# Performance work log

Measured on AMD Instinct MI355X. Metric: run time of the kernel, lower is better.

## Reference

```python
import math
import jax, jax.numpy as jnp
import numpy as np

DIM = 192
HEADS = 6
WIN = (16, 16)
N = WIN[0] * WIN[1]
B_ = 256
NW = 64
CPB_HIDDEN = 512


def _relative_coords_table(window_size):
    Wh, Ww = window_size
    h = np.arange(-(Wh - 1), Wh, dtype=np.float32)
    w = np.arange(-(Ww - 1), Ww, dtype=np.float32)
    table = np.stack(np.meshgrid(h, w, indexing='ij'), axis=-1)[None]  # (1, 2Wh-1, 2Ww-1, 2)
    table[..., 0] /= (Wh - 1)
    table[..., 1] /= (Ww - 1)
    table *= 8.0
    table = np.sign(table) * np.log2(np.abs(table) + 1.0) / np.log2(8.0)
    return table.astype(np.float32)


def _relative_position_index(window_size):
    Wh, Ww = window_size
    coords = np.stack(np.meshgrid(np.arange(Wh), np.arange(Ww), indexing='ij'))  # (2, Wh, Ww)
    flat = coords.reshape(2, -1)
    rel = flat[:, :, None] - flat[:, None, :]  # (2, N, N)
    rel = rel.transpose(1, 2, 0).astype(np.int64)
    rel[..., 0] += Wh - 1
    rel[..., 1] += Ww - 1
    rel[..., 0] *= 2 * Ww - 1
    return rel.sum(-1)  # (N, N)


def setup_inputs() -> dict:
    key = jax.random.key(0)
    ks = jax.random.split(key, 9)
    s = 1.0 / math.sqrt(DIM)
    inp = {
        'x': jax.random.normal(ks[0], (B_, N, DIM), dtype=jnp.float32),
        'mask': jax.random.normal(ks[1], (NW, N, N), dtype=jnp.float32),
        'qkv_w': jax.random.normal(ks[2], (3 * DIM, DIM), dtype=jnp.float32) * s,
        'qkv_b': jnp.zeros((3 * DIM,), dtype=jnp.float32),
        'proj_w': jax.random.normal(ks[3], (DIM, DIM), dtype=jnp.float32) * s,
        'proj_b': jnp.zeros((DIM,), dtype=jnp.float32),
        'logit_scale': jnp.full((HEADS, 1, 1), math.log(10.0), dtype=jnp.float32),
        'cpb_w1': jax.random.normal(ks[4], (CPB_HIDDEN, 2), dtype=jnp.float32) * (1.0 / math.sqrt(2.0)),
        'cpb_b1': jnp.zeros((CPB_HIDDEN,), dtype=jnp.float32),
        'cpb_w2': jax.random.normal(ks[5], (HEADS, CPB_HIDDEN), dtype=jnp.float32) * (1.0 / math.sqrt(CPB_HIDDEN)),
        'coords_table': jnp.asarray(_relative_coords_table(WIN)),
        'rel_index': jnp.asarray(_relative_position_index(WIN)),
    }
    return inp


def reference(x, mask, qkv_w, qkv_b, proj_w, proj_b, logit_scale,
              cpb_w1, cpb_b1, cpb_w2, coords_table, rel_index):
    Bw, n, C = x.shape
    H = logit_scale.shape[0]
    Dh = C // H
    eps = 1e-12

    qkv = x @ qkv_w.T + qkv_b                             # (B_, N, 3C)
    qkv = qkv.reshape(Bw, n, 3, H, Dh).transpose(2, 0, 3, 1, 4)
    q, k, v = qkv[0], qkv[1], qkv[2]                      # (B_, H, N, Dh)

    qn = q / jnp.maximum(jnp.linalg.norm(q, axis=-1, keepdims=True), eps)
    kn = k / jnp.maximum(jnp.linalg.norm(k, axis=-1, keepdims=True), eps)
    attn = jnp.einsum('bhnd,bhmd->bhnm', qn, kn)

    scale = jnp.exp(jnp.minimum(logit_scale, math.log(1.0 / 0.01)))  # (H,1,1)
    attn = attn * scale[None]

    # CPB MLP bias: (1, 2Wh-1, 2Ww-1, 2) -> (-1, H), gather, sigmoid-scale
    hbt = jax.nn.relu(coords_table @ cpb_w1.T + cpb_b1) @ cpb_w2.T   # (1, 2Wh-1, 2Ww-1, H)
    bias_table = hbt.reshape(-1, H)
    bias = bias_table[rel_index.reshape(-1)].reshape(n, n, H).transpose(2, 0, 1)
    attn = attn + 16.0 * jax.nn.sigmoid(bias)[None]

    nW = mask.shape[0]
    attn = attn.reshape(Bw // nW, nW, H, n, n) + mask[None, :, None]
    attn = attn.reshape(Bw, H, n, n)

    attn = jax.nn.softmax(attn, axis=-1)
    out = jnp.einsum('bhnm,bhmd->bhnd', attn, v)
    out = out.transpose(0, 2, 1, 3).reshape(Bw, n, C)
    return out @ proj_w.T + proj_b
```

## Files before the change

kernel.cpp:

```cpp
#include <hip/hip_runtime.h>

using bf16 = __bf16;
typedef bf16 bf16x4 __attribute__((ext_vector_type(4)));
typedef bf16 bf16x8 __attribute__((ext_vector_type(8)));
typedef float f32x4 __attribute__((ext_vector_type(4)));

__device__ __forceinline__ int swz192(int row, int col) {
  return row * 192 + (col ^ ((row & 7) << 3));
}
__device__ __forceinline__ int qk_idx(int row, int col) {
  return (row >> 1) * 64 + (row & 1) * 32 + (col ^ (((row >> 1) & 3) << 3));
}
__device__ __forceinline__ int vt_idx(int d, int n) {
  return d * 256 + (((n + ((d >> 3) << 4)) & 255) ^ ((d & 7) << 3));
}
__device__ __forceinline__ int p_idx4(int wv, int r, int c) {
  return wv * 1024 + r * 64 + (c ^ ((r & 7) << 3));
}

#define LOG2E 1.44269504088896f

template <bool A_BF16, bool OUT_F32, bool NORM_QK, int NT>
__global__ __launch_bounds__(256) void k_gemm(const void* __restrict__ Ap,
                                              const float* __restrict__ W,
                                              const float* __restrict__ bias,
                                              const float* __restrict__ lsc,
                                              void* __restrict__ Op, int Ntot) {
  __shared__ bf16 As[128 * 192];
  __shared__ bf16 Bs[64 * 192];
  const int bid = blockIdx.x;
  const int xcd = bid & 7;
  const int j = bid >> 3;
  const int m0 = (xcd + 8 * (j / NT)) * 128;
  const int n0 = (j % NT) * 64;
  const int t = threadIdx.x;

  if (A_BF16) {
    const bf16* A = (const bf16*)Ap;
#pragma unroll
    for (int i = 0; i < 12; ++i) {
      int f = t + i * 256;
      int row = f / 24, c8 = f % 24;
      bf16x8 v = *reinterpret_cast<const bf16x8*>(&A[(m0 + row) * 192 + c8 * 8]);
      *reinterpret_cast<bf16x8*>(&As[swz192(row, c8 * 8)]) = v;
    }
  } else {
    const float* A = (const float*)Ap;
#pragma unroll
    for (int i = 0; i < 24; ++i) {
      int f = t + i * 256;
      int row = f / 48, c4 = f % 48;
      f32x4 v = *reinterpret_cast<const f32x4*>(&A[(m0 + row) * 192 + c4 * 4]);
      bf16x4 hv;
      hv[0] = (bf16)v[0]; hv[1] = (bf16)v[1]; hv[2] = (bf16)v[2]; hv[3] = (bf16)v[3];
      *reinterpret_cast<bf16x4*>(&As[swz192(row, c4 * 4)]) = hv;
    }
  }
#pragma unroll
  for (int i = 0; i < 12; ++i) {
    int f = t + i * 256;
    int row = f / 48, c4 = f % 48;
    f32x4 v = *reinterpret_cast<const f32x4*>(&W[(n0 + row) * 192 + c4 * 4]);
    bf16x4 hv;
    hv[0] = (bf16)v[0]; hv[1] = (bf16)v[1]; hv[2] = (bf16)v[2]; hv[3] = (bf16)v[3];
    *reinterpret_cast<bf16x4*>(&Bs[swz192(row, c4 * 4)]) = hv;
  }
  __syncthreads();

  const int w = t >> 6, lane = t & 63, lo = lane & 15, hi = lane >> 4;
  const int wm = (w >> 1) * 64, wn = (w & 1) * 32;
  f32x4 acc[4][2];
#pragma unroll
  for (int a = 0; a < 4; ++a)
#pragma unroll
    for (int c = 0; c < 2; ++c) acc[a][c] = f32x4{0.f, 0.f, 0.f, 0.f};

#pragma unroll
  for (int ks = 0; ks < 6; ++ks) {
    const int k0 = ks * 32 + hi * 8;
    bf16x8 af[4], bfr[2];
#pragma unroll
    for (int ri = 0; ri < 4; ++ri)
      af[ri] = *reinterpret_cast<const bf16x8*>(&As[swz192(wm + ri * 16 + lo, k0)]);
#pragma unroll
    for (int ci = 0; ci < 2; ++ci)
      bfr[ci] = *reinterpret_cast<const bf16x8*>(&Bs[swz192(wn + ci * 16 + lo, k0)]);
#pragma unroll
    for (int ri = 0; ri < 4; ++ri)
#pragma unroll
      for (int ci = 0; ci < 2; ++ci)
        acc[ri][ci] = __builtin_amdgcn_mfma_f32_16x16x32_bf16(af[ri], bfr[ci], acc[ri][ci], 0, 0, 0);
  }

  if (NORM_QK) {
    const int cb = n0 + wn;
    const bool donorm = (cb < 384);
    float smul = 1.f;
    if (cb < 192)
      smul = expf(fminf(lsc[cb >> 5], 4.605170185988091f)) * LOG2E;
    const int col0 = cb + lo;
    const float b0 = bias[col0], b1 = bias[col0 + 16];
    bf16* O = (bf16*)Op;
#pragma unroll
    for (int ri = 0; ri < 4; ++ri)
#pragma unroll
      for (int rr = 0; rr < 4; ++rr) {
        float v0 = acc[ri][0][rr] + b0;
        float v1 = acc[ri][1][rr] + b1;
        if (donorm) {
          float ss = v0 * v0 + v1 * v1;
          ss += __shfl_xor(ss, 1, 16);
          ss += __shfl_xor(ss, 2, 16);
          ss += __shfl_xor(ss, 4, 16);
          ss += __shfl_xor(ss, 8, 16);
          const float rn = smul / fmaxf(sqrtf(ss), 1e-12f);
          v0 *= rn;
          v1 *= rn;
        }
        const int row = m0 + wm + ri * 16 + hi * 4 + rr;
        O[row * Ntot + col0] = (bf16)v0;
        O[row * Ntot + col0 + 16] = (bf16)v1;
      }
  } else {
#pragma unroll
    for (int ri = 0; ri < 4; ++ri)
#pragma unroll
      for (int ci = 0; ci < 2; ++ci) {
        const int col = n0 + wn + ci * 16 + lo;
        const float bv = bias[col];
#pragma unroll
        for (int rr = 0; rr < 4; ++rr) {
          const int row = m0 + wm + ri * 16 + hi * 4 + rr;
          const float val = acc[ri][ci][rr] + bv;
          if (OUT_F32)
            __builtin_nontemporal_store(val, &((float*)Op)[row * Ntot + col]);
          else
            ((bf16*)Op)[row * Ntot + col] = (bf16)val;
        }
      }
  }
}

__global__ void k_cpb1(const float* __restrict__ ct, const float* __restrict__ w1,
                       const float* __restrict__ b1, const float* __restrict__ w2,
                       float* __restrict__ bt) {
  int idx = blockIdx.x * 256 + threadIdx.x;
  if (idx >= 961 * 6) return;
  int r = idx / 6, hh = idx % 6;
  float t0 = ct[r * 2], t1 = ct[r * 2 + 1];
  float acc = 0.f;
  for (int j = 0; j < 512; ++j) {
    float hv = fmaf(w1[j * 2], t0, fmaf(w1[j * 2 + 1], t1, b1[j]));
    hv = fmaxf(hv, 0.f);
    acc = fmaf(hv, w2[hh * 512 + j], acc);
  }
  bt[idx] = acc;
}

__global__ void k_cpbT(const float* __restrict__ bt, const int* __restrict__ rel,
                       float* __restrict__ biasfT) {
  int idx = blockIdx.x * 256 + threadIdx.x;
  int hh = idx >> 16;
  int jj = (idx >> 8) & 255;
  int i = idx & 255;
  float v = bt[rel[i * 256 + jj] * 6 + hh];
  biasfT[idx] = LOG2E * 16.f / (1.f + expf(-v));
}

__global__ __launch_bounds__(256) void k_maskT(const float* __restrict__ m,
                                               bf16* __restrict__ o) {
  __shared__ float tile[64][65];
  const int mb = blockIdx.y;
  const int it = blockIdx.x >> 2, jt = blockIdx.x & 3;
  const int tx = threadIdx.x & 63, ty = threadIdx.x >> 6;
  const float* mp = m + mb * 65536;
#pragma unroll
  for (int rr = 0; rr < 16; ++rr)
    tile[rr * 4 + ty][tx] = mp[(it * 64 + rr * 4 + ty) * 256 + jt * 64 + tx];
  __syncthreads();
  bf16* op = o + mb * 65536;
#pragma unroll
  for (int rr = 0; rr < 16; ++rr)
    op[(jt * 64 + rr * 4 + ty) * 256 + it * 64 + tx] = (bf16)(LOG2E * tile[tx][rr * 4 + ty]);
}

__global__ __launch_bounds__(256) void k_attn(const bf16* __restrict__ qkv,
                                              const bf16* __restrict__ maskT,
                                              const float* __restrict__ biasfT,
                                              bf16* __restrict__ aout) {
  __shared__ bf16 ksh[256 * 32];
  __shared__ bf16 vts[32 * 256];
  __shared__ bf16 ps[4 * 16 * 64];

  const int bid = blockIdx.x;
  const int x = bid & 7, i = bid >> 3;
  const int mb = x * 8 + i / 24;
  const int rem = i % 24;
  const int b = (rem / 6) * 64 + mb;
  const int h = rem % 6;
  const int t = threadIdx.x;

  const int rsub = t >> 2;
  const int c4 = t & 3;
#pragma unroll
  for (int p = 0; p < 4; ++p) {
    const int row = p * 64 + rsub;
    const int base = (b * 256 + row) * 576 + h * 32 + c4 * 8;
    *reinterpret_cast<bf16x8*>(&ksh[qk_idx(row, c4 * 8)]) =
        *reinterpret_cast<const bf16x8*>(&qkv[base + 192]);
    bf16x8 v = *reinterpret_cast<const bf16x8*>(&qkv[base + 384]);
#pragma unroll
    for (int j = 0; j < 8; ++j) vts[vt_idx(c4 * 8 + j, row)] = v[j];
  }
  __syncthreads();

  const int w = t >> 6, lane = t & 63, lo = lane & 15, hi = lane >> 4;
  const float* bT = biasfT + (h << 16);
  const bf16* mT = maskT + (mb << 16);
  const bf16* qbase = qkv + (b * 256) * 576 + h * 32;

  bf16x8 afn = *reinterpret_cast<const bf16x8*>(&qbase[(w * 16 + lo) * 576 + hi * 8]);

  f32x4 bvp[4];
  bf16x4 mvp[4];
  {
    const int rbase0 = w * 16 + hi * 4;
#pragma unroll
    for (int c = 0; c < 4; ++c) {
      const int col = c * 16 + lo;
      bvp[c] = *reinterpret_cast<const f32x4*>(&bT[col * 256 + rbase0]);
      mvp[c] = *reinterpret_cast<const bf16x4*>(&mT[col * 256 + rbase0]);
    }
  }

  for (int rgi = 0; rgi < 4; ++rgi) {
    const int rg = rgi * 4 + w;
    const int rbase = rg * 16 + hi * 4;
    const bf16x8 af = afn;
    if (rgi < 3)
      afn = *reinterpret_cast<const bf16x8*>(&qbase[((rg + 4) * 16 + lo) * 576 + hi * 8]);

    f32x4 po0 = {0.f, 0.f, 0.f, 0.f}, po1 = {0.f, 0.f, 0.f, 0.f};
    float sum[4] = {0.f, 0.f, 0.f, 0.f};

#pragma unroll
    for (int ph = 0; ph < 4; ++ph) {
      f32x4 bv[4];
      bf16x4 mv[4];
#pragma unroll
      for (int c = 0; c < 4; ++c) { bv[c] = bvp[c]; mv[c] = mvp[c]; }
      if (ph < 3) {
#pragma unroll
        for (int c = 0; c < 4; ++c) {
          const int col = (ph + 1) * 64 + c * 16 + lo;
          bvp[c] = *reinterpret_cast<const f32x4*>(&bT[col * 256 + rbase]);
          mvp[c] = *reinterpret_cast<const bf16x4*>(&mT[col * 256 + rbase]);
        }
      } else if (rgi < 3) {
#pragma unroll
        for (int c = 0; c < 4; ++c) {
          const int col = c * 16 + lo;
          bvp[c] = *reinterpret_cast<const f32x4*>(&bT[col * 256 + rbase + 64]);
          mvp[c] = *reinterpret_cast<const bf16x4*>(&mT[col * 256 + rbase + 64]);
        }
      }
      bf16x8 kf[4];
#pragma unroll
      for (int c4i = 0; c4i < 4; ++c4i) {
        const int ct = ph * 4 + c4i;
        kf[c4i] = *reinterpret_cast<const bf16x8*>(&ksh[qk_idx(ct * 16 + lo, hi * 8)]);
      }
      f32x4 a[4];
#pragma unroll
      for (int c4i = 0; c4i < 4; ++c4i) {
        f32x4 z = {0.f, 0.f, 0.f, 0.f};
        a[c4i] = __builtin_amdgcn_mfma_f32_16x16x32_bf16(af, kf[c4i], z, 0, 0, 0);
      }
#pragma unroll
      for (int c4i = 0; c4i < 4; ++c4i)
#pragma unroll
        for (int rr = 0; rr < 4; ++rr) {
          const float s = a[c4i][rr] + bv[c4i][rr] + (float)mv[c4i][rr];
          const float p = exp2f(s);
          sum[rr] += p;
          ps[p_idx4(w, hi * 4 + rr, c4i * 16 + lo)] = (bf16)p;
        }
#pragma unroll
      for (int kb = 0; kb < 2; ++kb) {
        const bf16x8 pa = *reinterpret_cast<const bf16x8*>(&ps[p_idx4(w, lo, kb * 32 + hi * 8)]);
        const bf16x8 b0 = *reinterpret_cast<const bf16x8*>(&vts[vt_idx(lo, ph * 64 + kb * 32 + hi * 8)]);
        const bf16x8 b1 = *reinterpret_cast<const bf16x8*>(&vts[vt_idx(16 + lo, ph * 64 + kb * 32 + hi * 8)]);
        po0 = __builtin_amdgcn_mfma_f32_16x16x32_bf16(pa, b0, po0, 0, 0, 0);
        po1 = __builtin_amdgcn_mfma_f32_16x16x32_bf16(pa, b1, po1, 0, 0, 0);
      }
    }
#pragma unroll
    for (int rr = 0; rr < 4; ++rr) {
      float s = sum[rr];
      s += __shfl_xor(s, 1, 16);
      s += __shfl_xor(s, 2, 16);
      s += __shfl_xor(s, 4, 16);
      s += __shfl_xor(s, 8, 16);
      sum[rr] = 1.f / s;
    }
#pragma unroll
    for (int rr = 0; rr < 4; ++rr) {
      const int ob = (b * 256 + rbase + rr) * 192 + h * 32;
      aout[ob + lo] = (bf16)(po0[rr] * sum[rr]);
      aout[ob + 16 + lo] = (bf16)(po1[rr] * sum[rr]);
    }
  }
}

extern "C" void kernel_launch(void* const* d_in, const int* in_sizes, int n_in,
                              void* d_out, int out_size, void* d_ws, size_t ws_size,
                              hipStream_t stream) {
  const float* x      = (const float*)d_in[0];
  const float* mask   = (const float*)d_in[1];
  const float* qkv_w  = (const float*)d_in[2];
  const float* qkv_b  = (const float*)d_in[3];
  const float* proj_w = (const float*)d_in[4];
  const float* proj_b = (const float*)d_in[5];
  const float* lsc    = (const float*)d_in[6];
  const float* cpb_w1 = (const float*)d_in[7];
  const float* cpb_b1 = (const float*)d_in[8];
  const float* cpb_w2 = (const float*)d_in[9];
  const float* ctab   = (const float*)d_in[10];
  const int*   relidx = (const int*)d_in[11];

  char* ws = (char*)d_ws;
  bf16*  qkvb   = (bf16*)(ws);
  bf16*  aoutb  = (bf16*)(ws + 75497472);
  float* biasfT = (float*)(ws + 100663296);
  bf16*  maskTb = (bf16*)(ws + 102236160);
  float* bt     = (float*)(ws + 110624768);

  k_gemm<false, false, true, 9><<<4608, 256, 0, stream>>>(x, qkv_w, qkv_b, lsc, qkvb, 576);
  k_cpb1<<<23, 256, 0, stream>>>(ctab, cpb_w1, cpb_b1, cpb_w2, bt);
  k_cpbT<<<1536, 256, 0, stream>>>(bt, relidx, biasfT);
  k_maskT<<<dim3(16, 64), 256, 0, stream>>>(mask, maskTb);
  k_attn<<<1536, 256, 0, stream>>>(qkvb, maskTb, biasfT, aoutb);
  k_gemm<true, true, false, 3><<<1536, 256, 0, stream>>>(aoutb, proj_w, proj_b, nullptr,
                                                         (float*)d_out, 192);
}
```

Measured before the change: 225.9 us.

## Compute transposed scores with MFMA accumulator bias, drop mask/bias transposes, shrink GEMM tiles

The attention kernel now computes S^T via swapped MFMA operands and feeds bias plus mask in as the accumulator input, so the mask and bias tables can stay in natural row-major layout. The shared-memory transpose kernel for the mask is replaced by a simple elementwise conversion. Probability stores become vectorised bf16x4, and the row-sum reduction becomes a cross-lane shuffle. Separately, both GEMMs use 64-row M tiles instead of 128, doubling the grid. This trades less data reuse per block for more parallelism and lower LDS use.

```diff
diff --git a/kernel.cpp b/kernel.cpp
--- a/kernel.cpp
+++ b/kernel.cpp
@@ -26,19 +26,19 @@
                                               const float* __restrict__ bias,
                                               const float* __restrict__ lsc,
                                               void* __restrict__ Op, int Ntot) {
-  __shared__ bf16 As[128 * 192];
+  __shared__ bf16 As[64 * 192];
   __shared__ bf16 Bs[64 * 192];
   const int bid = blockIdx.x;
   const int xcd = bid & 7;
   const int j = bid >> 3;
-  const int m0 = (xcd + 8 * (j / NT)) * 128;
+  const int m0 = (xcd + 8 * (j / NT)) * 64;
   const int n0 = (j % NT) * 64;
   const int t = threadIdx.x;
 
   if (A_BF16) {
     const bf16* A = (const bf16*)Ap;
 #pragma unroll
-    for (int i = 0; i < 12; ++i) {
+    for (int i = 0; i < 6; ++i) {
       int f = t + i * 256;
       int row = f / 24, c8 = f % 24;
       bf16x8 v = *reinterpret_cast<const bf16x8*>(&A[(m0 + row) * 192 + c8 * 8]);
@@ -47,7 +47,7 @@
   } else {
     const float* A = (const float*)Ap;
 #pragma unroll
-    for (int i = 0; i < 24; ++i) {
+    for (int i = 0; i < 12; ++i) {
       int f = t + i * 256;
       int row = f / 48, c4 = f % 48;
       f32x4 v = *reinterpret_cast<const f32x4*>(&A[(m0 + row) * 192 + c4 * 4]);
@@ -68,25 +68,25 @@
   __syncthreads();
 
   const int w = t >> 6, lane = t & 63, lo = lane & 15, hi = lane >> 4;
-  const int wm = (w >> 1) * 64, wn = (w & 1) * 32;
-  f32x4 acc[4][2];
-#pragma unroll
-  for (int a = 0; a < 4; ++a)
+  const int wm = (w >> 1) * 32, wn = (w & 1) * 32;
+  f32x4 acc[2][2];
+#pragma unroll
+  for (int a = 0; a < 2; ++a)
 #pragma unroll
     for (int c = 0; c < 2; ++c) acc[a][c] = f32x4{0.f, 0.f, 0.f, 0.f};
 
 #pragma unroll
   for (int ks = 0; ks < 6; ++ks) {
     const int k0 = ks * 32 + hi * 8;
-    bf16x8 af[4], bfr[2];
-#pragma unroll
-    for (int ri = 0; ri < 4; ++ri)
+    bf16x8 af[2], bfr[2];
+#pragma unroll
+    for (int ri = 0; ri < 2; ++ri)
       af[ri] = *reinterpret_cast<const bf16x8*>(&As[swz192(wm + ri * 16 + lo, k0)]);
 #pragma unroll
     for (int ci = 0; ci < 2; ++ci)
       bfr[ci] = *reinterpret_cast<const bf16x8*>(&Bs[swz192(wn + ci * 16 + lo, k0)]);
 #pragma unroll
-    for (int ri = 0; ri < 4; ++ri)
+    for (int ri = 0; ri < 2; ++ri)
 #pragma unroll
       for (int ci = 0; ci < 2; ++ci)
         acc[ri][ci] = __builtin_amdgcn_mfma_f32_16x16x32_bf16(af[ri], bfr[ci], acc[ri][ci], 0, 0, 0);
@@ -102,7 +102,7 @@
     const float b0 = bias[col0], b1 = bias[col0 + 16];
     bf16* O = (bf16*)Op;
 #pragma unroll
-    for (int ri = 0; ri < 4; ++ri)
+    for (int ri = 0; ri < 2; ++ri)
 #pragma unroll
       for (int rr = 0; rr < 4; ++rr) {
         float v0 = acc[ri][0][rr] + b0;
@@ -123,7 +123,7 @@
       }
   } else {
 #pragma unroll
-    for (int ri = 0; ri < 4; ++ri)
+    for (int ri = 0; ri < 2; ++ri)
 #pragma unroll
       for (int ci = 0; ci < 2; ++ci) {
         const int col = n0 + wn + ci * 16 + lo;
@@ -157,36 +157,23 @@
   bt[idx] = acc;
 }
 
-__global__ void k_cpbT(const float* __restrict__ bt, const int* __restrict__ rel,
-                       float* __restrict__ biasfT) {
+__global__ void k_cpb2(const float* __restrict__ bt, const int* __restrict__ rel,
+                       float* __restrict__ biasf) {
   int idx = blockIdx.x * 256 + threadIdx.x;
   int hh = idx >> 16;
-  int jj = (idx >> 8) & 255;
-  int i = idx & 255;
-  float v = bt[rel[i * 256 + jj] * 6 + hh];
-  biasfT[idx] = LOG2E * 16.f / (1.f + expf(-v));
-}
-
-__global__ __launch_bounds__(256) void k_maskT(const float* __restrict__ m,
-                                               bf16* __restrict__ o) {
-  __shared__ float tile[64][65];
-  const int mb = blockIdx.y;
-  const int it = blockIdx.x >> 2, jt = blockIdx.x & 3;
-  const int tx = threadIdx.x & 63, ty = threadIdx.x >> 6;
-  const float* mp = m + mb * 65536;
-#pragma unroll
-  for (int rr = 0; rr < 16; ++rr)
-    tile[rr * 4 + ty][tx] = mp[(it * 64 + rr * 4 + ty) * 256 + jt * 64 + tx];
-  __syncthreads();
-  bf16* op = o + mb * 65536;
-#pragma unroll
-  for (int rr = 0; rr < 16; ++rr)
-    op[(jt * 64 + rr * 4 + ty) * 256 + it * 64 + tx] = (bf16)(LOG2E * tile[tx][rr * 4 + ty]);
+  int ij = idx & 65535;
+  float v = bt[rel[ij] * 6 + hh];
+  biasf[idx] = LOG2E * 16.f / (1.f + expf(-v));
+}
+
+__global__ void k_maskb(const float* __restrict__ m, bf16* __restrict__ o) {
+  int i = blockIdx.x * 256 + threadIdx.x;
+  o[i] = (bf16)(LOG2E * m[i]);
 }
 
 __global__ __launch_bounds__(256) void k_attn(const bf16* __restrict__ qkv,
-                                              const bf16* __restrict__ maskT,
-                                              const float* __restrict__ biasfT,
+                                              const bf16* __restrict__ maskb,
+                                              const float* __restrict__ biasf,
                                               bf16* __restrict__ aout) {
   __shared__ bf16 ksh[256 * 32];
   __shared__ bf16 vts[32 * 256];
@@ -201,67 +188,70 @@
   const int t = threadIdx.x;
 
   const int rsub = t >> 2;
-  const int c4 = t & 3;
+  const int c4s = t & 3;
 #pragma unroll
   for (int p = 0; p < 4; ++p) {
     const int row = p * 64 + rsub;
-    const int base = (b * 256 + row) * 576 + h * 32 + c4 * 8;
-    *reinterpret_cast<bf16x8*>(&ksh[qk_idx(row, c4 * 8)]) =
+    const int base = (b * 256 + row) * 576 + h * 32 + c4s * 8;
+    *reinterpret_cast<bf16x8*>(&ksh[qk_idx(row, c4s * 8)]) =
         *reinterpret_cast<const bf16x8*>(&qkv[base + 192]);
     bf16x8 v = *reinterpret_cast<const bf16x8*>(&qkv[base + 384]);
 #pragma unroll
-    for (int j = 0; j < 8; ++j) vts[vt_idx(c4 * 8 + j, row)] = v[j];
+    for (int jj = 0; jj < 8; ++jj) vts[vt_idx(c4s * 8 + jj, row)] = v[jj];
   }
   __syncthreads();
 
   const int w = t >> 6, lane = t & 63, lo = lane & 15, hi = lane >> 4;
-  const float* bT = biasfT + (h << 16);
-  const bf16* mT = maskT + (mb << 16);
+  const float* bT = biasf + (h << 16);
+  const bf16* mT = maskb + (mb << 16);
   const bf16* qbase = qkv + (b * 256) * 576 + h * 32;
+  const int kofs = 4 * hi;
 
   bf16x8 afn = *reinterpret_cast<const bf16x8*>(&qbase[(w * 16 + lo) * 576 + hi * 8]);
 
   f32x4 bvp[4];
   bf16x4 mvp[4];
   {
-    const int rbase0 = w * 16 + hi * 4;
+    const int qr0 = w * 16 + lo;
 #pragma unroll
     for (int c = 0; c < 4; ++c) {
-      const int col = c * 16 + lo;
-      bvp[c] = *reinterpret_cast<const f32x4*>(&bT[col * 256 + rbase0]);
-      mvp[c] = *reinterpret_cast<const bf16x4*>(&mT[col * 256 + rbase0]);
+      bvp[c] = *reinterpret_cast<const f32x4*>(&bT[qr0 * 256 + c * 16 + kofs]);
+      mvp[c] = *reinterpret_cast<const bf16x4*>(&mT[qr0 * 256 + c * 16 + kofs]);
     }
   }
 
   for (int rgi = 0; rgi < 4; ++rgi) {
     const int rg = rgi * 4 + w;
-    const int rbase = rg * 16 + hi * 4;
+    const int qrow = rg * 16 + lo;
     const bf16x8 af = afn;
     if (rgi < 3)
       afn = *reinterpret_cast<const bf16x8*>(&qbase[((rg + 4) * 16 + lo) * 576 + hi * 8]);
 
     f32x4 po0 = {0.f, 0.f, 0.f, 0.f}, po1 = {0.f, 0.f, 0.f, 0.f};
-    float sum[4] = {0.f, 0.f, 0.f, 0.f};
+    float psum = 0.f;
 
 #pragma unroll
     for (int ph = 0; ph < 4; ++ph) {
-      f32x4 bv[4];
-      bf16x4 mv[4];
-#pragma unroll
-      for (int c = 0; c < 4; ++c) { bv[c] = bvp[c]; mv[c] = mvp[c]; }
+      f32x4 cin[4];
+#pragma unroll
+      for (int c = 0; c < 4; ++c) {
+        cin[c][0] = bvp[c][0] + (float)mvp[c][0];
+        cin[c][1] = bvp[c][1] + (float)mvp[c][1];
+        cin[c][2] = bvp[c][2] + (float)mvp[c][2];
+        cin[c][3] = bvp[c][3] + (float)mvp[c][3];
+      }
       if (ph < 3) {
 #pragma unroll
         for (int c = 0; c < 4; ++c) {
-          const int col = (ph + 1) * 64 + c * 16 + lo;
-          bvp[c] = *reinterpret_cast<const f32x4*>(&bT[col * 256 + rbase]);
-          mvp[c] = *reinterpret_cast<const bf16x4*>(&mT[col * 256 + rbase]);
+          const int k0 = (ph + 1) * 64 + c * 16 + kofs;
+          bvp[c] = *reinterpret_cast<const f32x4*>(&bT[qrow * 256 + k0]);
+          mvp[c] = *reinterpret_cast<const bf16x4*>(&mT[qrow * 256 + k0]);
         }
       } else if (rgi < 3) {
 #pragma unroll
         for (int c = 0; c < 4; ++c) {
-          const int col = c * 16 + lo;
-          bvp[c] = *reinterpret_cast<const f32x4*>(&bT[col * 256 + rbase + 64]);
-          mvp[c] = *reinterpret_cast<const bf16x4*>(&mT[col * 256 + rbase + 64]);
+          bvp[c] = *reinterpret_cast<const f32x4*>(&bT[(qrow + 64) * 256 + c * 16 + kofs]);
+          mvp[c] = *reinterpret_cast<const bf16x4*>(&mT[(qrow + 64) * 256 + c * 16 + kofs]);
         }
       }
       bf16x8 kf[4];
@@ -272,19 +262,19 @@
       }
       f32x4 a[4];
 #pragma unroll
+      for (int c4i = 0; c4i < 4; ++c4i)
+        a[c4i] = __builtin_amdgcn_mfma_f32_16x16x32_bf16(kf[c4i], af, cin[c4i], 0, 0, 0);
+#pragma unroll
       for (int c4i = 0; c4i < 4; ++c4i) {
-        f32x4 z = {0.f, 0.f, 0.f, 0.f};
-        a[c4i] = __builtin_amdgcn_mfma_f32_16x16x32_bf16(af, kf[c4i], z, 0, 0, 0);
-      }
-#pragma unroll
-      for (int c4i = 0; c4i < 4; ++c4i)
+        bf16x4 hv;
 #pragma unroll
         for (int rr = 0; rr < 4; ++rr) {
-          const float s = a[c4i][rr] + bv[c4i][rr] + (float)mv[c4i][rr];
-          const float p = exp2f(s);
-          sum[rr] += p;
-          ps[p_idx4(w, hi * 4 + rr, c4i * 16 + lo)] = (bf16)p;
-        }
+          const float p = exp2f(a[c4i][rr]);
+          psum += p;
+          hv[rr] = (bf16)p;
+        }
+        *reinterpret_cast<bf16x4*>(&ps[p_idx4(w, lo, c4i * 16 + kofs)]) = hv;
+      }
 #pragma unroll
       for (int kb = 0; kb < 2; ++kb) {
         const bf16x8 pa = *reinterpret_cast<const bf16x8*>(&ps[p_idx4(w, lo, kb * 32 + hi * 8)]);
@@ -294,20 +284,17 @@
         po1 = __builtin_amdgcn_mfma_f32_16x16x32_bf16(pa, b1, po1, 0, 0, 0);
       }
     }
+    float s = psum;
+    s += __shfl_xor(s, 16, 64);
+    s += __shfl_xor(s, 32, 64);
+    s = 1.f / s;
+    const int rbase = rg * 16 + hi * 4;
 #pragma unroll
     for (int rr = 0; rr < 4; ++rr) {
-      float s = sum[rr];
-      s += __shfl_xor(s, 1, 16);
-      s += __shfl_xor(s, 2, 16);
-      s += __shfl_xor(s, 4, 16);
-      s += __shfl_xor(s, 8, 16);
-      sum[rr] = 1.f / s;
-    }
-#pragma unroll
-    for (int rr = 0; rr < 4; ++rr) {
+      const float rs = __shfl(s, 4 * hi + rr, 64);
       const int ob = (b * 256 + rbase + rr) * 192 + h * 32;
-      aout[ob + lo] = (bf16)(po0[rr] * sum[rr]);
-      aout[ob + 16 + lo] = (bf16)(po1[rr] * sum[rr]);
+      aout[ob + lo] = (bf16)(po0[rr] * rs);
+      aout[ob + 16 + lo] = (bf16)(po1[rr] * rs);
     }
   }
 }
@@ -329,17 +316,17 @@
   const int*   relidx = (const int*)d_in[11];
 
   char* ws = (char*)d_ws;
-  bf16*  qkvb   = (bf16*)(ws);
-  bf16*  aoutb  = (bf16*)(ws + 75497472);
-  float* biasfT = (float*)(ws + 100663296);
-  bf16*  maskTb = (bf16*)(ws + 102236160);
-  float* bt     = (float*)(ws + 110624768);
-
-  k_gemm<false, false, true, 9><<<4608, 256, 0, stream>>>(x, qkv_w, qkv_b, lsc, qkvb, 576);
+  bf16*  qkvb  = (bf16*)(ws);
+  bf16*  aoutb = (bf16*)(ws + 75497472);
+  float* biasf = (float*)(ws + 100663296);
+  bf16*  maskb = (bf16*)(ws + 102236160);
+  float* bt    = (float*)(ws + 110624768);
+
+  k_gemm<false, false, true, 9><<<9216, 256, 0, stream>>>(x, qkv_w, qkv_b, lsc, qkvb, 576);
   k_cpb1<<<23, 256, 0, stream>>>(ctab, cpb_w1, cpb_b1, cpb_w2, bt);
-  k_cpbT<<<1536, 256, 0, stream>>>(bt, relidx, biasfT);
-  k_maskT<<<dim3(16, 64), 256, 0, stream>>>(mask, maskTb);
-  k_attn<<<1536, 256, 0, stream>>>(qkvb, maskTb, biasfT, aoutb);
-  k_gemm<true, true, false, 3><<<1536, 256, 0, stream>>>(aoutb, proj_w, proj_b, nullptr,
+  k_cpb2<<<1536, 256, 0, stream>>>(bt, relidx, biasf);
+  k_maskb<<<16384, 256, 0, stream>>>(mask, maskb);
+  k_attn<<<1536, 256, 0, stream>>>(qkvb, maskb, biasf, aoutb);
+  k_gemm<true, true, false, 3><<<3072, 256, 0, stream>>>(aoutb, proj_w, proj_b, nullptr,
                                                          (float*)d_out, 192);
 }
```

Measured after the change: 234.7 us. +3.9%, slower.

## Pre-convert inputs and weights to bf16 and halve GEMM M-tile

Applied to the files above, without the earlier changes.

Adds a separate conversion kernel that casts x, qkv_w and proj_w to bf16 once, so both GEMMs load bf16 operands directly instead of converting fp32 in every tile. The GEMM M-tile shrinks from 128 to 64 rows, which doubles the grid size and cuts LDS and register use per block. The cost is an extra full pass over x, writing a bf16 copy and reading it back, plus three more launches. The smaller tiles also re-read the weight tile more often.

```diff
diff --git a/kernel.cpp b/kernel.cpp
--- a/kernel.cpp
+++ b/kernel.cpp
@@ -20,73 +20,67 @@
 
 #define LOG2E 1.44269504088896f
 
-template <bool A_BF16, bool OUT_F32, bool NORM_QK, int NT>
-__global__ __launch_bounds__(256) void k_gemm(const void* __restrict__ Ap,
-                                              const float* __restrict__ W,
+__global__ void k_conv8(const float* __restrict__ in, bf16* __restrict__ o) {
+  const int i = (blockIdx.x * 256 + threadIdx.x) * 8;
+  const f32x4 a = *reinterpret_cast<const f32x4*>(&in[i]);
+  const f32x4 b = *reinterpret_cast<const f32x4*>(&in[i + 4]);
+  bf16x8 v;
+  v[0] = (bf16)a[0]; v[1] = (bf16)a[1]; v[2] = (bf16)a[2]; v[3] = (bf16)a[3];
+  v[4] = (bf16)b[0]; v[5] = (bf16)b[1]; v[6] = (bf16)b[2]; v[7] = (bf16)b[3];
+  *reinterpret_cast<bf16x8*>(&o[i]) = v;
+}
+
+template <bool OUT_F32, bool NORM_QK, int NT>
+__global__ __launch_bounds__(256) void k_gemm(const bf16* __restrict__ A,
+                                              const bf16* __restrict__ W,
                                               const float* __restrict__ bias,
                                               const float* __restrict__ lsc,
                                               void* __restrict__ Op, int Ntot) {
-  __shared__ bf16 As[128 * 192];
+  __shared__ bf16 As[64 * 192];
   __shared__ bf16 Bs[64 * 192];
   const int bid = blockIdx.x;
   const int xcd = bid & 7;
   const int j = bid >> 3;
-  const int m0 = (xcd + 8 * (j / NT)) * 128;
+  const int m0 = (xcd + 8 * (j / NT)) * 64;
   const int n0 = (j % NT) * 64;
   const int t = threadIdx.x;
 
-  if (A_BF16) {
-    const bf16* A = (const bf16*)Ap;
-#pragma unroll
-    for (int i = 0; i < 12; ++i) {
-      int f = t + i * 256;
-      int row = f / 24, c8 = f % 24;
-      bf16x8 v = *reinterpret_cast<const bf16x8*>(&A[(m0 + row) * 192 + c8 * 8]);
-      *reinterpret_cast<bf16x8*>(&As[swz192(row, c8 * 8)]) = v;
-    }
-  } else {
-    const float* A = (const float*)Ap;
-#pragma unroll
-    for (int i = 0; i < 24; ++i) {
-      int f = t + i * 256;
-      int row = f / 48, c4 = f % 48;
-      f32x4 v = *reinterpret_cast<const f32x4*>(&A[(m0 + row) * 192 + c4 * 4]);
-      bf16x4 hv;
-      hv[0] = (bf16)v[0]; hv[1] = (bf16)v[1]; hv[2] = (bf16)v[2]; hv[3] = (bf16)v[3];
-      *reinterpret_cast<bf16x4*>(&As[swz192(row, c4 * 4)]) = hv;
-    }
-  }
-#pragma unroll
-  for (int i = 0; i < 12; ++i) {
+#pragma unroll
+  for (int i = 0; i < 6; ++i) {
     int f = t + i * 256;
-    int row = f / 48, c4 = f % 48;
-    f32x4 v = *reinterpret_cast<const f32x4*>(&W[(n0 + row) * 192 + c4 * 4]);
-    bf16x4 hv;
-    hv[0] = (bf16)v[0]; hv[1] = (bf16)v[1]; hv[2] = (bf16)v[2]; hv[3] = (bf16)v[3];
-    *reinterpret_cast<bf16x4*>(&Bs[swz192(row, c4 * 4)]) = hv;
+    int row = f / 24, c8 = f % 24;
+    bf16x8 v = *reinterpret_cast<const bf16x8*>(&A[(m0 + row) * 192 + c8 * 8]);
+    *reinterpret_cast<bf16x8*>(&As[swz192(row, c8 * 8)]) = v;
+  }
+#pragma unroll
+  for (int i = 0; i < 6; ++i) {
+    int f = t + i * 256;
+    int row = f / 24, c8 = f % 24;
+    bf16x8 v = *reinterpret_cast<const bf16x8*>(&W[(n0 + row) * 192 + c8 * 8]);
+    *reinterpret_cast<bf16x8*>(&Bs[swz192(row, c8 * 8)]) = v;
   }
   __syncthreads();
 
   const int w = t >> 6, lane = t & 63, lo = lane & 15, hi = lane >> 4;
-  const int wm = (w >> 1) * 64, wn = (w & 1) * 32;
-  f32x4 acc[4][2];
-#pragma unroll
-  for (int a = 0; a < 4; ++a)
+  const int wm = (w >> 1) * 32, wn = (w & 1) * 32;
+  f32x4 acc[2][2];
+#pragma unroll
+  for (int a = 0; a < 2; ++a)
 #pragma unroll
     for (int c = 0; c < 2; ++c) acc[a][c] = f32x4{0.f, 0.f, 0.f, 0.f};
 
 #pragma unroll
   for (int ks = 0; ks < 6; ++ks) {
     const int k0 = ks * 32 + hi * 8;
-    bf16x8 af[4], bfr[2];
-#pragma unroll
-    for (int ri = 0; ri < 4; ++ri)
+    bf16x8 af[2], bfr[2];
+#pragma unroll
+    for (int ri = 0; ri < 2; ++ri)
       af[ri] = *reinterpret_cast<const bf16x8*>(&As[swz192(wm + ri * 16 + lo, k0)]);
 #pragma unroll
     for (int ci = 0; ci < 2; ++ci)
       bfr[ci] = *reinterpret_cast<const bf16x8*>(&Bs[swz192(wn + ci * 16 + lo, k0)]);
 #pragma unroll
-    for (int ri = 0; ri < 4; ++ri)
+    for (int ri = 0; ri < 2; ++ri)
 #pragma unroll
       for (int ci = 0; ci < 2; ++ci)
         acc[ri][ci] = __builtin_amdgcn_mfma_f32_16x16x32_bf16(af[ri], bfr[ci], acc[ri][ci], 0, 0, 0);
@@ -102,7 +96,7 @@
     const float b0 = bias[col0], b1 = bias[col0 + 16];
     bf16* O = (bf16*)Op;
 #pragma unroll
-    for (int ri = 0; ri < 4; ++ri)
+    for (int ri = 0; ri < 2; ++ri)
 #pragma unroll
       for (int rr = 0; rr < 4; ++rr) {
         float v0 = acc[ri][0][rr] + b0;
@@ -123,7 +117,7 @@
       }
   } else {
 #pragma unroll
-    for (int ri = 0; ri < 4; ++ri)
+    for (int ri = 0; ri < 2; ++ri)
 #pragma unroll
       for (int ci = 0; ci < 2; ++ci) {
         const int col = n0 + wn + ci * 16 + lo;
@@ -201,16 +195,16 @@
   const int t = threadIdx.x;
 
   const int rsub = t >> 2;
-  const int c4 = t & 3;
+  const int c4s = t & 3;
 #pragma unroll
   for (int p = 0; p < 4; ++p) {
     const int row = p * 64 + rsub;
-    const int base = (b * 256 + row) * 576 + h * 32 + c4 * 8;
-    *reinterpret_cast<bf16x8*>(&ksh[qk_idx(row, c4 * 8)]) =
+    const int base = (b * 256 + row) * 576 + h * 32 + c4s * 8;
+    *reinterpret_cast<bf16x8*>(&ksh[qk_idx(row, c4s * 8)]) =
         *reinterpret_cast<const bf16x8*>(&qkv[base + 192]);
     bf16x8 v = *reinterpret_cast<const bf16x8*>(&qkv[base + 384]);
 #pragma unroll
-    for (int j = 0; j < 8; ++j) vts[vt_idx(c4 * 8 + j, row)] = v[j];
+    for (int jj = 0; jj < 8; ++jj) vts[vt_idx(c4s * 8 + jj, row)] = v[jj];
   }
   __syncthreads();
 
@@ -330,16 +324,22 @@
 
   char* ws = (char*)d_ws;
   bf16*  qkvb   = (bf16*)(ws);
+  bf16*  xb     = (bf16*)(ws + 75497472);
   bf16*  aoutb  = (bf16*)(ws + 75497472);
   float* biasfT = (float*)(ws + 100663296);
   bf16*  maskTb = (bf16*)(ws + 102236160);
   float* bt     = (float*)(ws + 110624768);
-
-  k_gemm<false, false, true, 9><<<4608, 256, 0, stream>>>(x, qkv_w, qkv_b, lsc, qkvb, 576);
+  bf16*  qkv_wb = (bf16*)(ws + 110647840);
+  bf16*  proj_wb= (bf16*)(ws + 110869024);
+
+  k_conv8<<<6144, 256, 0, stream>>>(x, xb);
+  k_conv8<<<54, 256, 0, stream>>>(qkv_w, qkv_wb);
+  k_conv8<<<18, 256, 0, stream>>>(proj_w, proj_wb);
+  k_gemm<false, true, 9><<<9216, 256, 0, stream>>>(xb, qkv_wb, qkv_b, lsc, qkvb, 576);
   k_cpb1<<<23, 256, 0, stream>>>(ctab, cpb_w1, cpb_b1, cpb_w2, bt);
   k_cpbT<<<1536, 256, 0, stream>>>(bt, relidx, biasfT);
   k_maskT<<<dim3(16, 64), 256, 0, stream>>>(mask, maskTb);
   k_attn<<<1536, 256, 0, stream>>>(qkvb, maskTb, biasfT, aoutb);
-  k_gemm<true, true, false, 3><<<1536, 256, 0, stream>>>(aoutb, proj_w, proj_b, nullptr,
-                                                         (float*)d_out, 192);
-}
+  k_gemm<true, false, 3><<<3072, 256, 0, stream>>>(aoutb, proj_wb, proj_b, nullptr,
+                                                   (float*)d_out, 192);
+}
```

Result: no change. 222.0 us (-1.7%).
